# Performance work log

Measured on AMD Instinct MI355X. Metric: run time of the kernel, lower is better.

The kernel has to match this reference:

```python
import jax, jax.numpy as jnp
import numpy as np

B, S, DIM = 2, 2048, 1024
N_HEADS, HEAD_DIM = 16, 64
ROPE_THETA = 10000.0


def _rope_cos_sin(seq_len, head_dim, dtype=jnp.float32):
    inv_freq = 1.0 / (ROPE_THETA ** (jnp.arange(0, head_dim, 2, dtype=jnp.float32) / head_dim))
    ang = jnp.arange(seq_len, dtype=jnp.float32)[:, None] * inv_freq[None, :]  # [S, D/2]
    return jnp.cos(ang).astype(dtype), jnp.sin(ang).astype(dtype)


def _apply_rope(t, cos, sin):
    # t: [B, S, H, D]; cos/sin: [S, D/2]
    t1 = t[..., 0::2]
    t2 = t[..., 1::2]
    c = cos[None, :, None, :]
    s = sin[None, :, None, :]
    r1 = t1 * c - t2 * s
    r2 = t1 * s + t2 * c
    # interleave back to original even/odd layout
    return jnp.stack([r1, r2], axis=-1).reshape(t.shape)


def setup_inputs() -> dict:
    key = jax.random.key(0)
    ks = jax.random.split(key, 5)
    scale = 1.0 / np.sqrt(DIM)
    return {
        "x": jax.random.normal(ks[0], (B, S, DIM), dtype=jnp.float32),
        "Wq": jax.random.normal(ks[1], (DIM, DIM), dtype=jnp.float32) * scale,
        "Wk": jax.random.normal(ks[2], (DIM, DIM), dtype=jnp.float32) * scale,
        "Wv": jax.random.normal(ks[3], (DIM, DIM), dtype=jnp.float32) * scale,
        "Wo": jax.random.normal(ks[4], (DIM, DIM), dtype=jnp.float32) * scale,
    }


def reference(x, Wq, Wk, Wv, Wo):
    b, s, _ = x.shape
    q = (x @ Wq.T).reshape(b, s, N_HEADS, HEAD_DIM)
    k = (x @ Wk.T).reshape(b, s, N_HEADS, HEAD_DIM)
    v = (x @ Wv.T).reshape(b, s, N_HEADS, HEAD_DIM)

    cos, sin = _rope_cos_sin(s, HEAD_DIM, dtype=q.dtype)
    q = _apply_rope(q, cos, sin)
    k = _apply_rope(k, cos, sin)

    # [B, H, S, S] scores with causal mask
    attn = jnp.einsum("bqhd,bkhd->bhqk", q, k) / np.sqrt(HEAD_DIM)
    causal = jnp.tril(jnp.ones((s, s), dtype=bool))
    attn = jnp.where(causal[None, None], attn, jnp.float32(-jnp.inf))
    probs = jax.nn.softmax(attn.astype(jnp.float32), axis=-1).astype(q.dtype)

    out = jnp.einsum("bhqk,bkhd->bqhd", probs, v).reshape(b, s, N_HEADS * HEAD_DIM)
    return out @ Wo.T
```

## Files before the change

### kernel.cpp

```cpp
#include <hip/hip_runtime.h>
#include <hip/hip_bf16.h>

#define S_LEN 2048
#define DIMSZ 1024
#define NH    16
#define HD    64

typedef __attribute__((ext_vector_type(8))) short short8v;
typedef __attribute__((ext_vector_type(4))) short short4v;
typedef __attribute__((ext_vector_type(4))) float f32x4;

typedef const __attribute__((address_space(1))) unsigned GU;
typedef __attribute__((address_space(3))) unsigned LU;

__device__ __forceinline__ void gl16(const ushort* g, ushort* l) {
  __builtin_amdgcn_global_load_lds((GU*)g, (LU*)l, 16, 0, 0);
}

__device__ __forceinline__ ushort f2bf(float f) {
  union { float f; unsigned u; } v; v.f = f;
  unsigned u = v.u;
  return (ushort)((u + 0x7FFFu + ((u >> 16) & 1u)) >> 16);
}

__device__ __forceinline__ uint cvtpk(float lo, float hi) {
  uint d;
  asm("v_cvt_pk_bf16_f32 %0, %1, %2" : "=v"(d) : "v"(lo), "v"(hi));
  return d;
}

__global__ __launch_bounds__(256) void cvt_k(
    const float* __restrict__ x, const float* __restrict__ wq,
    const float* __restrict__ wk, const float* __restrict__ wv,
    const float* __restrict__ wo,
    ushort* __restrict__ xb, ushort* __restrict__ wqkvb, ushort* __restrict__ wob)
{
  size_t gid = (size_t)blockIdx.x * 256 + threadIdx.x;
  size_t e0 = gid * 8;
  const float* src; ushort* dst;
  if (e0 < (4u << 20)) { src = x + e0; dst = xb + e0; }
  else if (e0 < (7u << 20)) {
    size_t o = e0 - (4u << 20);
    const float* w = (o < (1u << 20)) ? wq : ((o < (2u << 20)) ? wk : wv);
    src = w + (o & ((1u << 20) - 1)); dst = wqkvb + o;
  } else {
    size_t o = e0 - (7u << 20);
    src = wo + o; dst = wob + o;
  }
  float4 a = *(const float4*)src;
  float4 b = *(const float4*)(src + 4);
  short8v h;
  h[0] = (short)f2bf(a.x); h[1] = (short)f2bf(a.y);
  h[2] = (short)f2bf(a.z); h[3] = (short)f2bf(a.w);
  h[4] = (short)f2bf(b.x); h[5] = (short)f2bf(b.y);
  h[6] = (short)f2bf(b.z); h[7] = (short)f2bf(b.w);
  *(short8v*)dst = h;
}

__global__ __launch_bounds__(256) void rope_table_k(float2* __restrict__ tab) {
  int i = blockIdx.x * 256 + threadIdx.x;
  int f = i >> 11, s = i & (S_LEN - 1);
  float inv = powf(10000.f, -(float)f * (1.f / 32.f));
  float ang = (float)s * inv;
  tab[i] = make_float2(cosf(ang), sinf(ang));
}

#define QSTAGE(c, kt_) do {                                                     \
    int k0_ = (kt_) * 64;                                                       \
    _Pragma("unroll")                                                           \
    for (int j_ = 0; j_ < 4; ++j_) {                                            \
      int R_ = w * 32 + j_ * 8;                                                 \
      gl16(xb + (size_t)(bm + R_ + r8) * DIMSZ + k0_ + cswz, &lA[c][R_ * 64]);  \
      gl16(W  + (size_t)(bn + R_ + r8) * DIMSZ + k0_ + cswz, &lB[c][R_ * 64]);  \
    }                                                                           \
  } while (0)

__global__ __launch_bounds__(256) void gemm_qkv_k(
    const ushort* __restrict__ xb, const ushort* __restrict__ wqkvb,
    ushort* __restrict__ qb, ushort* __restrict__ kb, ushort* __restrict__ vtb,
    const float2* __restrict__ rtab)
{
  __shared__ ushort lA[2][128 * 64];
  __shared__ ushort lB[2][128 * 64];
  const int t = threadIdx.x;
  int id = blockIdx.x;
  int nid = (id & 7) * 96 + (id >> 3);
  const int which = nid >> 8;
  const int bm = ((nid >> 3) & 31) * 128, bn = (nid & 7) * 128;
  const ushort* W = wqkvb + ((size_t)which << 20);
  const int w = t >> 6, l = t & 63, lr = l & 15, lg = l >> 4;
  const int wm = (w >> 1) * 64, wn = (w & 1) * 64;
  const int r8 = l >> 3;
  const int cswz = ((l & 7) ^ r8) * 8;

  f32x4 acc[4][4] = {};

  QSTAGE(0, 0);
  for (int kt = 0; kt < DIMSZ / 64; ++kt) {
    const int cur = kt & 1;
    if (kt + 1 < DIMSZ / 64) {
      QSTAGE(cur ^ 1, kt + 1);
      asm volatile("s_waitcnt vmcnt(8)" ::: "memory");
    } else {
      asm volatile("s_waitcnt vmcnt(0)" ::: "memory");
    }
    __builtin_amdgcn_s_barrier();
    asm volatile("" ::: "memory");
    #pragma unroll
    for (int kk = 0; kk < 2; ++kk) {
      short8v a[4], b[4];
      #pragma unroll
      for (int mt = 0; mt < 4; ++mt) {
        int row = wm + mt * 16 + lr;
        a[mt] = *(const short8v*)((const char*)lA[cur] + row * 128 + ((kk * 64 + lg * 16) ^ ((row & 7) << 4)));
      }
      #pragma unroll
      for (int nt = 0; nt < 4; ++nt) {
        int row = wn + nt * 16 + lr;
        b[nt] = *(const short8v*)((const char*)lB[cur] + row * 128 + ((kk * 64 + lg * 16) ^ ((row & 7) << 4)));
      }
      #pragma unroll
      for (int mt = 0; mt < 4; ++mt)
        #pragma unroll
        for (int nt = 0; nt < 4; ++nt)
          acc[mt][nt] = __builtin_amdgcn_mfma_f32_16x16x32_bf16(b[nt], a[mt], acc[mt][nt], 0, 0, 0);
    }
    __builtin_amdgcn_s_barrier();
    asm volatile("" ::: "memory");
  }

  const int bb = bm >> 11, s_base = bm & (S_LEN - 1);

  if (which == 2) {
    ushort* tb = &lA[0][0];
    #pragma unroll
    for (int mt = 0; mt < 4; ++mt)
      #pragma unroll
      for (int nt = 0; nt < 4; ++nt)
        #pragma unroll
        for (int r = 0; r < 4; ++r) {
          int row = wn + nt * 16 + lg * 4 + r;
          int col = wm + mt * 16 + lr;
          int byte = row * 256 + ((col * 2) ^ (((row >> 2) & 3) << 5));
          *(ushort*)((char*)tb + byte) = f2bf(acc[mt][nt][r]);
        }
    __syncthreads();
    int row = t >> 1, half = t & 1;
    int h = (bn + row) >> 6, d = (bn + row) & 63;
    ushort* vdst = vtb + ((size_t)(bb * NH + h) * HD + d) * S_LEN + s_base + half * 64;
    #pragma unroll
    for (int j = 0; j < 8; ++j) {
      int byte = row * 256 + ((half * 128 + j * 16) ^ (((row >> 2) & 3) << 5));
      *(short8v*)(vdst + j * 8) = *(const short8v*)((const char*)tb + byte);
    }
  } else {
    ushort* dst = (which == 0) ? qb : kb;
    const float QS = (which == 0) ? (0.125f * 1.4426950408889634f) : 1.0f;
    #pragma unroll
    for (int mt = 0; mt < 4; ++mt) {
      int s = s_base + wm + mt * 16 + lr;
      #pragma unroll
      for (int nt = 0; nt < 4; ++nt) {
        int nw = bn + wn + nt * 16 + lg * 4;
        int h = nw >> 6, d0 = nw & 63;
        uint pk[2];
        #pragma unroll
        for (int rp = 0; rp < 2; ++rp) {
          float2 cs = rtab[(d0 >> 1) * S_LEN + rp * S_LEN + s];
          float t1 = acc[mt][nt][2 * rp], t2 = acc[mt][nt][2 * rp + 1];
          float o0 = (t1 * cs.x - t2 * cs.y) * QS;
          float o1 = (t1 * cs.y + t2 * cs.x) * QS;
          pk[rp] = (uint)f2bf(o0) | ((uint)f2bf(o1) << 16);
        }
        uint2 pv; pv.x = pk[0]; pv.y = pk[1];
        *(uint2*)(dst + ((size_t)(bb * NH + h) * S_LEN + s) * HD + d0) = pv;
      }
    }
  }
}

template<bool DIAG>
__device__ __forceinline__ void attn_tile(
    const ushort* lK, const ushort* lV, ushort* lPw,
    const short8v* qf, f32x4* o, float& m2, float& lsum,
    int lr, int lg, int wrow)
{
  f32x4 sacc[4] = {};
  __builtin_amdgcn_s_setprio(1);
  #pragma unroll
  for (int kk = 0; kk < 2; ++kk)
    #pragma unroll
    for (int jt = 0; jt < 4; ++jt) {
      int row = jt * 16 + lr;
      short8v kf = *(const short8v*)((const char*)lK + row * 128 + ((kk * 64 + lg * 16) ^ ((row & 7) << 4)));
      sacc[jt] = __builtin_amdgcn_mfma_f32_16x16x32_bf16(kf, qf[kk], sacc[jt], 0, 0, 0);
    }
  __builtin_amdgcn_s_setprio(0);

  float v2[4][4];
  #pragma unroll
  for (int jt = 0; jt < 4; ++jt)
    #pragma unroll
    for (int r = 0; r < 4; ++r) {
      float sv = sacc[jt][r];
      if (DIAG && (jt * 16 + lg * 4 + r > wrow + lr)) sv = -3e38f;
      v2[jt][r] = sv;
    }
  float mj[4];
  #pragma unroll
  for (int jt = 0; jt < 4; ++jt)
    mj[jt] = fmaxf(fmaxf(v2[jt][0], v2[jt][1]), fmaxf(v2[jt][2], v2[jt][3]));
  float pmax = fmaxf(fmaxf(mj[0], mj[1]), fmaxf(mj[2], mj[3]));

  const bool need = __any(pmax > m2 + 8.f);
  float mn = m2;
  float so = 1.f;
  if (need) {
    float rmax = pmax;
    rmax = fmaxf(rmax, __shfl_xor(rmax, 16));
    rmax = fmaxf(rmax, __shfl_xor(rmax, 32));
    mn = fmaxf(m2, rmax);
    so = exp2f(m2 - mn);
    m2 = mn;
  }
  float pe[4][4];
  float ps = 0.f;
  #pragma unroll
  for (int jt = 0; jt < 4; ++jt)
    #pragma unroll
    for (int r = 0; r < 4; ++r) {
      pe[jt][r] = exp2f(v2[jt][r] - mn);
      ps += pe[jt][r];
    }
  if (need) {
    lsum = lsum * so + ps;
    #pragma unroll
    for (int r = 0; r < 4; ++r) {
      float sor = __shfl(so, lg * 4 + r);
      #pragma unroll
      for (int dt = 0; dt < 4; ++dt) o[dt][r] *= sor;
    }
  } else {
    lsum += ps;
  }
  #pragma unroll
  for (int jt = 0; jt < 4; ++jt) {
    uint2 pv;
    pv.x = cvtpk(pe[jt][0], pe[jt][1]);
    pv.y = cvtpk(pe[jt][2], pe[jt][3]);
    *(uint2*)((char*)lPw + lr * 128 + ((jt * 32 + lg * 8) ^ ((lr & 7) << 4))) = pv;
  }
  __builtin_amdgcn_s_setprio(1);
  #pragma unroll
  for (int kk = 0; kk < 2; ++kk) {
    short8v pa = *(const short8v*)((const char*)lPw + lr * 128 + ((kk * 64 + lg * 16) ^ ((lr & 7) << 4)));
    #pragma unroll
    for (int dt = 0; dt < 4; ++dt) {
      int row = dt * 16 + lr;
      short8v vb = *(const short8v*)((const char*)lV + row * 128 + ((kk * 64 + lg * 16) ^ ((row & 7) << 4)));
      o[dt] = __builtin_amdgcn_mfma_f32_16x16x32_bf16(pa, vb, o[dt], 0, 0, 0);
    }
  }
  __builtin_amdgcn_s_setprio(0);
}

__device__ __forceinline__ void store_tile(
    ushort* __restrict__ ab, int bh, int qt, int w, int lr, int lg,
    const f32x4* o, float lsum)
{
  float lf = lsum;
  lf += __shfl_xor(lf, 16);
  lf += __shfl_xor(lf, 32);
  int b = bh >> 4, h = bh & 15;
  #pragma unroll
  for (int r = 0; r < 4; ++r) {
    float li = __shfl(lf, lg * 4 + r);
    float inv = 1.f / li;
    int qg = qt * 64 + w * 16 + lg * 4 + r;
    #pragma unroll
    for (int dt = 0; dt < 4; ++dt)
      ab[((size_t)b * S_LEN + qg) * DIMSZ + h * HD + dt * 16 + lr] = f2bf(o[dt][r] * inv);
  }
}

#define STAGE(c, ktile) do {                                                  \
    int kk0_ = (ktile) * 64;                                                  \
    _Pragma("unroll")                                                         \
    for (int j_ = 0; j_ < 2; ++j_) {                                          \
      int R_ = w * 16 + j_ * 8;                                               \
      gl16(kbh + (size_t)(kk0_ + R_ + r8) * HD + cswz, &lKb[c][R_ * 64]);     \
      gl16(vbh + (size_t)(R_ + r8) * S_LEN + kk0_ + cswz, &lVb[c][R_ * 64]);  \
    }                                                                         \
  } while (0)

__global__ __launch_bounds__(256, 4) void flash_k(
    const ushort* __restrict__ qb, const ushort* __restrict__ kb,
    const ushort* __restrict__ vtb, ushort* __restrict__ ab)
{
  __shared__ ushort lKb[2][64 * 64];
  __shared__ ushort lVb[2][64 * 64];
  __shared__ ushort lP[4][16 * 64];

  int id = blockIdx.x;
  int nid = (id & 7) * 128 + (id >> 3);
  const int bh = (nid >> 7) * 4 + (nid & 3);
  const int qt = 31 - ((nid & 127) >> 2);
  const int NT = qt + 1;

  const int t = threadIdx.x, w = t >> 6, l = t & 63, lr = l & 15, lg = l >> 4;
  const int r8 = l >> 3;
  const int cswz = ((l & 7) ^ r8) * 8;
  const ushort* kbh = kb + (size_t)bh * S_LEN * HD;
  const ushort* vbh = vtb + (size_t)bh * HD * S_LEN;

  short8v qf[2];
  #pragma unroll
  for (int kk = 0; kk < 2; ++kk)
    qf[kk] = *(const short8v*)(qb + ((size_t)bh * S_LEN + qt * 64 + w * 16 + lr) * HD + kk * 32 + lg * 8);

  float m2 = -3e38f, lsum = 0.f;
  f32x4 o[4] = {};

  STAGE(0, 0);
  asm volatile("s_waitcnt vmcnt(0)" ::: "memory");
  __builtin_amdgcn_s_barrier();
  asm volatile("" ::: "memory");

  for (int kt = 0; kt < NT; ++kt) {
    const int cur = kt & 1;
    if (kt + 1 < NT) STAGE(cur ^ 1, kt + 1);
    const ushort* lK = lKb[cur];
    const ushort* lV = lVb[cur];
    if (kt == qt) attn_tile<true >(lK, lV, lP[w], qf, o, m2, lsum, lr, lg, w * 16);
    else          attn_tile<false>(lK, lV, lP[w], qf, o, m2, lsum, lr, lg, w * 16);
    asm volatile("s_waitcnt vmcnt(0)" ::: "memory");
    __builtin_amdgcn_s_barrier();
    asm volatile("" ::: "memory");
  }

  store_tile(ab, bh, qt, w, lr, lg, o, lsum);
}

#define OSTAGE(c, kt_) do {                                                     \
    int k0_ = (kt_) * 64;                                                       \
    _Pragma("unroll")                                                           \
    for (int j_ = 0; j_ < 4; ++j_) {                                            \
      int R_ = w * 32 + j_ * 8;                                                 \
      gl16(ab  + (size_t)(bm + R_ + r8) * DIMSZ + k0_ + cswz, &lA[c][R_ * 64]); \
      gl16(wob + (size_t)(bn + R_ + r8) * DIMSZ + k0_ + cswz, &lB[c][R_ * 64]); \
    }                                                                           \
  } while (0)

__global__ __launch_bounds__(256) void gemm_out_k(
    const ushort* __restrict__ ab, const ushort* __restrict__ wob, float* __restrict__ out)
{
  __shared__ ushort lA[2][128 * 64];
  __shared__ ushort lB[2][128 * 64];
  const int t = threadIdx.x;
  int id = blockIdx.x;
  int nid = (id & 7) * 32 + (id >> 3);
  const int bm = (nid >> 3) * 128, bn = (nid & 7) * 128;
  const int w = t >> 6, l = t & 63, lr = l & 15, lg = l >> 4;
  const int wm = (w >> 1) * 64, wn = (w & 1) * 64;
  const int r8 = l >> 3;
  const int cswz = ((l & 7) ^ r8) * 8;

  f32x4 acc[4][4] = {};

  OSTAGE(0, 0);
  for (int kt = 0; kt < DIMSZ / 64; ++kt) {
    const int cur = kt & 1;
    if (kt + 1 < DIMSZ / 64) {
      OSTAGE(cur ^ 1, kt + 1);
      asm volatile("s_waitcnt vmcnt(8)" ::: "memory");
    } else {
      asm volatile("s_waitcnt vmcnt(0)" ::: "memory");
    }
    __builtin_amdgcn_s_barrier();
    asm volatile("" ::: "memory");
    #pragma unroll
    for (int kk = 0; kk < 2; ++kk) {
      short8v a[4], b[4];
      #pragma unroll
      for (int mt = 0; mt < 4; ++mt) {
        int row = wm + mt * 16 + lr;
        a[mt] = *(const short8v*)((const char*)lA[cur] + row * 128 + ((kk * 64 + lg * 16) ^ ((row & 7) << 4)));
      }
      #pragma unroll
      for (int nt = 0; nt < 4; ++nt) {
        int row = wn + nt * 16 + lr;
        b[nt] = *(const short8v*)((const char*)lB[cur] + row * 128 + ((kk * 64 + lg * 16) ^ ((row & 7) << 4)));
      }
      #pragma unroll
      for (int mt = 0; mt < 4; ++mt)
        #pragma unroll
        for (int nt = 0; nt < 4; ++nt)
          acc[mt][nt] = __builtin_amdgcn_mfma_f32_16x16x32_bf16(b[nt], a[mt], acc[mt][nt], 0, 0, 0);
    }
    __builtin_amdgcn_s_barrier();
    asm volatile("" ::: "memory");
  }

  #pragma unroll
  for (int mt = 0; mt < 4; ++mt) {
    int m = bm + wm + mt * 16 + lr;
    #pragma unroll
    for (int nt = 0; nt < 4; ++nt) {
      int nb = bn + wn + nt * 16 + lg * 4;
      *(f32x4*)(out + (size_t)m * DIMSZ + nb) = acc[mt][nt];
    }
  }
}

extern "C" void kernel_launch(void* const* d_in, const int* in_sizes, int n_in,
                              void* d_out, int out_size, void* d_ws, size_t ws_size,
                              hipStream_t stream) {
  (void)in_sizes; (void)n_in; (void)out_size; (void)ws_size;
  const float* x  = (const float*)d_in[0];
  const float* Wq = (const float*)d_in[1];
  const float* Wk = (const float*)d_in[2];
  const float* Wv = (const float*)d_in[3];
  const float* Wo = (const float*)d_in[4];
  float* out = (float*)d_out;

  char* ws = (char*)d_ws;
  ushort* qb    = (ushort*)(ws);
  ushort* kb    = (ushort*)(ws + ((size_t)8  << 20));
  ushort* vtb   = (ushort*)(ws + ((size_t)16 << 20));
  ushort* xb    = (ushort*)(ws + ((size_t)24 << 20));
  ushort* ab    = xb;
  ushort* wqkvb = (ushort*)(ws + ((size_t)32 << 20));
  ushort* wob   = (ushort*)(ws + ((size_t)38 << 20));
  float2* rtab  = (float2*)(ws + ((size_t)40 << 20));

  hipLaunchKernelGGL(cvt_k, dim3(4096), dim3(256), 0, stream,
                     x, Wq, Wk, Wv, Wo, xb, wqkvb, wob);
  hipLaunchKernelGGL(rope_table_k, dim3(S_LEN * 32 / 256), dim3(256), 0, stream, rtab);
  hipLaunchKernelGGL(gemm_qkv_k, dim3(768), dim3(256), 0, stream,
                     xb, wqkvb, qb, kb, vtb, rtab);
  hipLaunchKernelGGL(flash_k, dim3(1024), dim3(256), 0, stream, qb, kb, vtb, ab);
  hipLaunchKernelGGL(gemm_out_k, dim3(256), dim3(256), 0, stream, ab, wob, out);
}
```

Before: 122.7 us.

## Rewrite flash attention with 32x32 MFMA, 128-row query tiles, and register-resident P

The flash attention kernel now has each block handle 128 query rows, with each wave owning 32 rows, using 32x32x16 bf16 MFMAs instead of 16x16x32. The P matrix stays in registers, rearranged with v_permlane32_swap, so the LDS round trip for probabilities is gone. Sub-tiles above the causal diagonal are skipped per wave. This halves the grid to 512 blocks and amortizes each K/V tile load over twice as many queries. The trade-offs are higher register pressure and fewer blocks, which may hurt occupancy and load balance.

```diff
diff --git a/kernel.cpp b/kernel.cpp
--- a/kernel.cpp
+++ b/kernel.cpp
@@ -9,6 +9,7 @@
 typedef __attribute__((ext_vector_type(8))) short short8v;
 typedef __attribute__((ext_vector_type(4))) short short4v;
 typedef __attribute__((ext_vector_type(4))) float f32x4;
+typedef __attribute__((ext_vector_type(16))) float f32x16;
 
 typedef const __attribute__((address_space(1))) unsigned GU;
 typedef __attribute__((address_space(3))) unsigned LU;
@@ -27,6 +28,10 @@
   uint d;
   asm("v_cvt_pk_bf16_f32 %0, %1, %2" : "=v"(d) : "v"(lo), "v"(hi));
   return d;
+}
+
+__device__ __forceinline__ void pl32swap(uint& a, uint& b) {
+  asm volatile("v_permlane32_swap_b32 %0, %1" : "+v"(a), "+v"(b));
 }
 
 __global__ __launch_bounds__(256) void cvt_k(
@@ -179,110 +184,6 @@
   }
 }
 
-template<bool DIAG>
-__device__ __forceinline__ void attn_tile(
-    const ushort* lK, const ushort* lV, ushort* lPw,
-    const short8v* qf, f32x4* o, float& m2, float& lsum,
-    int lr, int lg, int wrow)
-{
-  f32x4 sacc[4] = {};
-  __builtin_amdgcn_s_setprio(1);
-  #pragma unroll
-  for (int kk = 0; kk < 2; ++kk)
-    #pragma unroll
-    for (int jt = 0; jt < 4; ++jt) {
-      int row = jt * 16 + lr;
-      short8v kf = *(const short8v*)((const char*)lK + row * 128 + ((kk * 64 + lg * 16) ^ ((row & 7) << 4)));
-      sacc[jt] = __builtin_amdgcn_mfma_f32_16x16x32_bf16(kf, qf[kk], sacc[jt], 0, 0, 0);
-    }
-  __builtin_amdgcn_s_setprio(0);
-
-  float v2[4][4];
-  #pragma unroll
-  for (int jt = 0; jt < 4; ++jt)
-    #pragma unroll
-    for (int r = 0; r < 4; ++r) {
-      float sv = sacc[jt][r];
-      if (DIAG && (jt * 16 + lg * 4 + r > wrow + lr)) sv = -3e38f;
-      v2[jt][r] = sv;
-    }
-  float mj[4];
-  #pragma unroll
-  for (int jt = 0; jt < 4; ++jt)
-    mj[jt] = fmaxf(fmaxf(v2[jt][0], v2[jt][1]), fmaxf(v2[jt][2], v2[jt][3]));
-  float pmax = fmaxf(fmaxf(mj[0], mj[1]), fmaxf(mj[2], mj[3]));
-
-  const bool need = __any(pmax > m2 + 8.f);
-  float mn = m2;
-  float so = 1.f;
-  if (need) {
-    float rmax = pmax;
-    rmax = fmaxf(rmax, __shfl_xor(rmax, 16));
-    rmax = fmaxf(rmax, __shfl_xor(rmax, 32));
-    mn = fmaxf(m2, rmax);
-    so = exp2f(m2 - mn);
-    m2 = mn;
-  }
-  float pe[4][4];
-  float ps = 0.f;
-  #pragma unroll
-  for (int jt = 0; jt < 4; ++jt)
-    #pragma unroll
-    for (int r = 0; r < 4; ++r) {
-      pe[jt][r] = exp2f(v2[jt][r] - mn);
-      ps += pe[jt][r];
-    }
-  if (need) {
-    lsum = lsum * so + ps;
-    #pragma unroll
-    for (int r = 0; r < 4; ++r) {
-      float sor = __shfl(so, lg * 4 + r);
-      #pragma unroll
-      for (int dt = 0; dt < 4; ++dt) o[dt][r] *= sor;
-    }
-  } else {
-    lsum += ps;
-  }
-  #pragma unroll
-  for (int jt = 0; jt < 4; ++jt) {
-    uint2 pv;
-    pv.x = cvtpk(pe[jt][0], pe[jt][1]);
-    pv.y = cvtpk(pe[jt][2], pe[jt][3]);
-    *(uint2*)((char*)lPw + lr * 128 + ((jt * 32 + lg * 8) ^ ((lr & 7) << 4))) = pv;
-  }
-  __builtin_amdgcn_s_setprio(1);
-  #pragma unroll
-  for (int kk = 0; kk < 2; ++kk) {
-    short8v pa = *(const short8v*)((const char*)lPw + lr * 128 + ((kk * 64 + lg * 16) ^ ((lr & 7) << 4)));
-    #pragma unroll
-    for (int dt = 0; dt < 4; ++dt) {
-      int row = dt * 16 + lr;
-      short8v vb = *(const short8v*)((const char*)lV + row * 128 + ((kk * 64 + lg * 16) ^ ((row & 7) << 4)));
-      o[dt] = __builtin_amdgcn_mfma_f32_16x16x32_bf16(pa, vb, o[dt], 0, 0, 0);
-    }
-  }
-  __builtin_amdgcn_s_setprio(0);
-}
-
-__device__ __forceinline__ void store_tile(
-    ushort* __restrict__ ab, int bh, int qt, int w, int lr, int lg,
-    const f32x4* o, float lsum)
-{
-  float lf = lsum;
-  lf += __shfl_xor(lf, 16);
-  lf += __shfl_xor(lf, 32);
-  int b = bh >> 4, h = bh & 15;
-  #pragma unroll
-  for (int r = 0; r < 4; ++r) {
-    float li = __shfl(lf, lg * 4 + r);
-    float inv = 1.f / li;
-    int qg = qt * 64 + w * 16 + lg * 4 + r;
-    #pragma unroll
-    for (int dt = 0; dt < 4; ++dt)
-      ab[((size_t)b * S_LEN + qg) * DIMSZ + h * HD + dt * 16 + lr] = f2bf(o[dt][r] * inv);
-  }
-}
-
 #define STAGE(c, ktile) do {                                                  \
     int kk0_ = (ktile) * 64;                                                  \
     _Pragma("unroll")                                                         \
@@ -299,46 +200,167 @@
 {
   __shared__ ushort lKb[2][64 * 64];
   __shared__ ushort lVb[2][64 * 64];
-  __shared__ ushort lP[4][16 * 64];
 
   int id = blockIdx.x;
-  int nid = (id & 7) * 128 + (id >> 3);
-  const int bh = (nid >> 7) * 4 + (nid & 3);
-  const int qt = 31 - ((nid & 127) >> 2);
-  const int NT = qt + 1;
-
-  const int t = threadIdx.x, w = t >> 6, l = t & 63, lr = l & 15, lg = l >> 4;
+  int nid = (id & 7) * 64 + (id >> 3);
+  const int bh = (nid >> 6) * 4 + (nid & 3);
+  const int qi = 15 - ((nid & 63) >> 2);
+  const int NT = 2 * qi + 2;
+
+  const int t = threadIdx.x, w = t >> 6, l = t & 63;
+  const int l31 = l & 31, hi = l >> 5;
   const int r8 = l >> 3;
   const int cswz = ((l & 7) ^ r8) * 8;
   const ushort* kbh = kb + (size_t)bh * S_LEN * HD;
   const ushort* vbh = vtb + (size_t)bh * HD * S_LEN;
 
-  short8v qf[2];
+  const int qrow = 128 * qi + 32 * w + l31;
+  short8v qf[4];
   #pragma unroll
-  for (int kk = 0; kk < 2; ++kk)
-    qf[kk] = *(const short8v*)(qb + ((size_t)bh * S_LEN + qt * 64 + w * 16 + lr) * HD + kk * 32 + lg * 8);
+  for (int ks = 0; ks < 4; ++ks)
+    qf[ks] = *(const short8v*)(qb + ((size_t)bh * S_LEN + qrow) * HD + ks * 16 + hi * 8);
 
   float m2 = -3e38f, lsum = 0.f;
-  f32x4 o[4] = {};
+  f32x16 o0 = {}, o1 = {};
 
   STAGE(0, 0);
   asm volatile("s_waitcnt vmcnt(0)" ::: "memory");
   __builtin_amdgcn_s_barrier();
   asm volatile("" ::: "memory");
+
+  const int wqmax = 128 * qi + 32 * w + 31;
+  const int wqmin = wqmax - 31;
 
   for (int kt = 0; kt < NT; ++kt) {
     const int cur = kt & 1;
     if (kt + 1 < NT) STAGE(cur ^ 1, kt + 1);
     const ushort* lK = lKb[cur];
     const ushort* lV = lVb[cur];
-    if (kt == qt) attn_tile<true >(lK, lV, lP[w], qf, o, m2, lsum, lr, lg, w * 16);
-    else          attn_tile<false>(lK, lV, lP[w], qf, o, m2, lsum, lr, lg, w * 16);
+    const int kbase = kt * 64;
+    const bool skip0 = kbase > wqmax;
+    const bool skip1 = kbase + 32 > wqmax;
+
+    if (!skip0) {
+      f32x16 sacc0 = {}, sacc1 = {};
+      __builtin_amdgcn_s_setprio(1);
+      #pragma unroll
+      for (int ks = 0; ks < 4; ++ks) {
+        short8v kf = *(const short8v*)((const char*)lK + l31 * 128 + ((ks * 32 + hi * 16) ^ ((l31 & 7) << 4)));
+        sacc0 = __builtin_amdgcn_mfma_f32_32x32x16_bf16(kf, qf[ks], sacc0, 0, 0, 0);
+      }
+      if (!skip1) {
+        #pragma unroll
+        for (int ks = 0; ks < 4; ++ks) {
+          int row = 32 + l31;
+          short8v kf = *(const short8v*)((const char*)lK + row * 128 + ((ks * 32 + hi * 16) ^ ((row & 7) << 4)));
+          sacc1 = __builtin_amdgcn_mfma_f32_32x32x16_bf16(kf, qf[ks], sacc1, 0, 0, 0);
+        }
+      }
+      __builtin_amdgcn_s_setprio(0);
+
+      float pm = -3e38f;
+      const bool nm0 = (kbase + 31 > wqmin);
+      #pragma unroll
+      for (int r = 0; r < 16; ++r) {
+        int kk = kbase + (r & 3) + 8 * (r >> 2) + 4 * hi;
+        float v = sacc0[r];
+        if (nm0 && (kk > qrow)) v = -3e38f;
+        sacc0[r] = v;
+        pm = fmaxf(pm, v);
+      }
+      if (!skip1) {
+        const bool nm1 = (kbase + 63 > wqmin);
+        #pragma unroll
+        for (int r = 0; r < 16; ++r) {
+          int kk = kbase + 32 + (r & 3) + 8 * (r >> 2) + 4 * hi;
+          float v = sacc1[r];
+          if (nm1 && (kk > qrow)) v = -3e38f;
+          sacc1[r] = v;
+          pm = fmaxf(pm, v);
+        }
+      }
+
+      const bool need = __any(pm > m2 + 8.f);
+      float mn = m2, so = 1.f;
+      if (need) {
+        float rmax = fmaxf(pm, __shfl_xor(pm, 32));
+        mn = fmaxf(m2, rmax);
+        so = exp2f(m2 - mn);
+        m2 = mn;
+      }
+
+      float ps = 0.f;
+      short8v pa[4];
+      #pragma unroll
+      for (int s = 0; s < 2; ++s) {
+        float e[8];
+        #pragma unroll
+        for (int j = 0; j < 8; ++j) { e[j] = exp2f(sacc0[8 * s + j] - mn); ps += e[j]; }
+        uint a0 = cvtpk(e[0], e[1]), b0 = cvtpk(e[4], e[5]);
+        uint a1 = cvtpk(e[2], e[3]), b1 = cvtpk(e[6], e[7]);
+        pl32swap(a0, b0); pl32swap(a1, b1);
+        union { short8v v; uint u[4]; } pu;
+        pu.u[0] = a0; pu.u[1] = a1; pu.u[2] = b0; pu.u[3] = b1;
+        pa[s] = pu.v;
+      }
+      if (!skip1) {
+        #pragma unroll
+        for (int s = 0; s < 2; ++s) {
+          float e[8];
+          #pragma unroll
+          for (int j = 0; j < 8; ++j) { e[j] = exp2f(sacc1[8 * s + j] - mn); ps += e[j]; }
+          uint a0 = cvtpk(e[0], e[1]), b0 = cvtpk(e[4], e[5]);
+          uint a1 = cvtpk(e[2], e[3]), b1 = cvtpk(e[6], e[7]);
+          pl32swap(a0, b0); pl32swap(a1, b1);
+          union { short8v v; uint u[4]; } pu;
+          pu.u[0] = a0; pu.u[1] = a1; pu.u[2] = b0; pu.u[3] = b1;
+          pa[2 + s] = pu.v;
+        }
+      } else {
+        short8v z = {};
+        pa[2] = z; pa[3] = z;
+      }
+
+      if (need) {
+        lsum = lsum * so + ps;
+        #pragma unroll
+        for (int r = 0; r < 16; ++r) {
+          float soq = __shfl(so, (r & 3) + 8 * (r >> 2) + 4 * hi);
+          o0[r] *= soq; o1[r] *= soq;
+        }
+      } else {
+        lsum += ps;
+      }
+
+      __builtin_amdgcn_s_setprio(1);
+      #pragma unroll
+      for (int ks = 0; ks < 4; ++ks) {
+        short8v vf0 = *(const short8v*)((const char*)lV + l31 * 128 + ((ks * 32 + hi * 16) ^ ((l31 & 7) << 4)));
+        o0 = __builtin_amdgcn_mfma_f32_32x32x16_bf16(pa[ks], vf0, o0, 0, 0, 0);
+        int row = 32 + l31;
+        short8v vf1 = *(const short8v*)((const char*)lV + row * 128 + ((ks * 32 + hi * 16) ^ ((row & 7) << 4)));
+        o1 = __builtin_amdgcn_mfma_f32_32x32x16_bf16(pa[ks], vf1, o1, 0, 0, 0);
+      }
+      __builtin_amdgcn_s_setprio(0);
+    }
+
     asm volatile("s_waitcnt vmcnt(0)" ::: "memory");
     __builtin_amdgcn_s_barrier();
     asm volatile("" ::: "memory");
   }
 
-  store_tile(ab, bh, qt, w, lr, lg, o, lsum);
+  float lf = lsum + __shfl_xor(lsum, 32);
+  float inv = 1.f / lf;
+  const int b = bh >> 4, h = bh & 15;
+  #pragma unroll
+  for (int r = 0; r < 16; ++r) {
+    int qloc = (r & 3) + 8 * (r >> 2) + 4 * hi;
+    float invq = __shfl(inv, qloc);
+    int qg = 128 * qi + 32 * w + qloc;
+    ushort* dst = ab + ((size_t)b * S_LEN + qg) * DIMSZ + h * HD;
+    dst[l31]      = f2bf(o0[r] * invq);
+    dst[32 + l31] = f2bf(o1[r] * invq);
+  }
 }
 
 #define OSTAGE(c, kt_) do {                                                     \
@@ -438,6 +460,6 @@
   hipLaunchKernelGGL(rope_table_k, dim3(S_LEN * 32 / 256), dim3(256), 0, stream, rtab);
   hipLaunchKernelGGL(gemm_qkv_k, dim3(768), dim3(256), 0, stream,
                      xb, wqkvb, qb, kb, vtb, rtab);
-  hipLaunchKernelGGL(flash_k, dim3(1024), dim3(256), 0, stream, qb, kb, vtb, ab);
+  hipLaunchKernelGGL(flash_k, dim3(512), dim3(256), 0, stream, qb, kb, vtb, ab);
   hipLaunchKernelGGL(gemm_out_k, dim3(256), dim3(256), 0, stream, ab, wob, out);
 }
```

After: 143.9 us. +17.2%, slower.
